# Kernel optimization log

Hardware: AMD Instinct MI355X
Metric: run time of the kernel (lower is better)

Reference implementation:

```python
import jax, jax.numpy as jnp
import numpy as np

EPS = 1e-20

def squash(s):
    # n = ||s||; out = (1 - 1/(exp(n)+eps)) * s/(n+eps)
    n = jnp.linalg.norm(s, axis=-1, keepdims=True)
    return (1.0 - 1.0 / (jnp.exp(n) + EPS)) * (s / (n + EPS))

def setup_inputs() -> dict:
    key = jax.random.key(0)
    k1, k2 = jax.random.split(key)
    B, K, J, I, Z = 128, 32, 1152, 8, 16
    x = jax.random.normal(k1, (B, J, I), dtype=jnp.float32)
    # kaiming_normal_ fan_in init for W
    W = jax.random.normal(k2, (K, J, I, Z), dtype=jnp.float32) * np.float32(np.sqrt(2.0 / (J * I)))
    b = jnp.zeros((K, J, 1), dtype=jnp.float32)
    return {"x": x, "W": W, "b": b}

def reference(x, W, b):
    Z = W.shape[-1]
    # capsule transform: u[b,k,j,z] = sum_i x[b,j,i] * W[k,j,i,z]
    u = jnp.einsum('bji,kjiz->bkjz', x, W)
    # self-similarity: c[b,k,i] = sum_{j,z} u[b,k,i,z]*u[b,k,j,z]
    #                            = sum_z u[b,k,i,z] * (sum_j u[b,k,j,z])
    c = jnp.einsum('bkjz,bkz->bkj', u, u.sum(axis=2))[..., None]
    c = c / jnp.sqrt(jnp.asarray(Z, dtype=u.dtype))
    c = jax.nn.softmax(c, axis=1) + b  # softmax over caps2 (K) axis
    s = jnp.sum(u * c, axis=-2)  # [B, K, Z]
    return squash(s)
```

## Files before the change

kernel.cpp:

```cpp
#include <hip/hip_runtime.h>
#include <hip/hip_bf16.h>
#include <math.h>

#define BB 128
#define KK 32
#define JJ 1152
#define II 8
#define ZZ 16

#define NJSA 48
#define NJT  144

typedef __attribute__((ext_vector_type(8))) short short8;
typedef __attribute__((ext_vector_type(4))) float floatx4;

#define N_USUM  (KK * BB * ZZ)
#define N_USUMP (NJSA * KK * BB * ZZ)
#define N_SACCP ((size_t)NJT * KK * BB * ZZ)

__device__ __forceinline__ float bf2f(short h) {
    unsigned int w = ((unsigned int)(unsigned short)h) << 16;
    float f; __builtin_memcpy(&f, &w, 4);
    return f;
}

extern "C" __global__ __launch_bounds__(256)
void kX(const float* __restrict__ x, __hip_bfloat16* __restrict__ xbf) {
    int idx = blockIdx.x * 256 + threadIdx.x;
    int j_in = idx & 15;
    int rest = idx >> 4;
    int b    = rest & 127;
    int j    = (rest >> 7) * 16 + j_in;
    const float4* xp = (const float4*)(x + ((size_t)b * JJ + j) * II);
    float4 a = xp[0], c = xp[1];
    union { short8 v; __hip_bfloat16 h[8]; } u;
    u.h[0] = __float2bfloat16(a.x); u.h[1] = __float2bfloat16(a.y);
    u.h[2] = __float2bfloat16(a.z); u.h[3] = __float2bfloat16(a.w);
    u.h[4] = __float2bfloat16(c.x); u.h[5] = __float2bfloat16(c.y);
    u.h[6] = __float2bfloat16(c.z); u.h[7] = __float2bfloat16(c.w);
    *(short8*)(xbf + ((size_t)j * BB + b) * II) = u.v;
}

extern "C" __global__ __launch_bounds__(256)
void kW(const float* __restrict__ W, __hip_bfloat16* __restrict__ Wt) {
    int idx = blockIdx.x * 256 + threadIdx.x;
    int z    = idx & 15;
    int rest = idx >> 4;
    int j    = rest % JJ;
    int k    = rest / JJ;
    const float* src = W + (((size_t)k * JJ + j) * II) * ZZ + z;
    union { short8 v; __hip_bfloat16 h[8]; } u;
#pragma unroll
    for (int i = 0; i < II; ++i) u.h[i] = __float2bfloat16(src[i * ZZ]);
    *(short8*)(Wt + (((size_t)k * JJ + j) * ZZ + z) * II) = u.v;
}

extern "C" __global__ __launch_bounds__(64)
void kA(const __hip_bfloat16* __restrict__ xbf,
        const __hip_bfloat16* __restrict__ Wt, float* __restrict__ usum_p) {
    const int kt = blockIdx.x;
    const int bt = blockIdx.y;
    const int js = blockIdx.z;
    const int l  = threadIdx.x;
    const int n  = l & 15;
    const int g  = l >> 4;
    const int b  = bt * 16 + n;

    short8 xv[6];
#pragma unroll
    for (int q = 0; q < 6; ++q) {
        int j = (js * 6 + q) * 4 + g;
        xv[q] = *(const short8*)(xbf + ((size_t)j * BB + b) * II);
    }

    floatx4 acc[4];
#pragma unroll
    for (int kk = 0; kk < 4; ++kk) acc[kk] = (floatx4){0.f, 0.f, 0.f, 0.f};

#pragma unroll
    for (int kk = 0; kk < 4; ++kk) {
        const int k = kt * 4 + kk;
#pragma unroll
        for (int q = 0; q < 6; ++q) {
            int j = (js * 6 + q) * 4 + g;
            short8 a = *(const short8*)(Wt + (((size_t)k * JJ + j) * ZZ + n) * II);
            acc[kk] = __builtin_amdgcn_mfma_f32_16x16x32_bf16(a, xv[q], acc[kk], 0, 0, 0);
        }
    }
#pragma unroll
    for (int kk = 0; kk < 4; ++kk) {
        const int k = kt * 4 + kk;
        *(floatx4*)(usum_p + (((size_t)js * KK + k) * BB + b) * ZZ + g * 4) = acc[kk];
    }
}

extern "C" __global__ __launch_bounds__(256)
void kR(const float* __restrict__ usum_p, float* __restrict__ usum) {
    int idx = blockIdx.x * 256 + threadIdx.x;
    floatx4 s = (floatx4){0.f, 0.f, 0.f, 0.f};
#pragma unroll 8
    for (int js = 0; js < NJSA; ++js)
        s += *(const floatx4*)(usum_p + (size_t)js * N_USUM + (size_t)idx * 4);
    *(floatx4*)(usum + (size_t)idx * 4) = s;
}

extern "C" __global__ __launch_bounds__(256)
void kBC(const __hip_bfloat16* __restrict__ xbf,
         const __hip_bfloat16* __restrict__ Wt,
         const float* __restrict__ usum, const float* __restrict__ bias,
         float* __restrict__ sacc_p) {
    __shared__ float eS[KK * 8 * 16];
    __shared__ float Sw[4 * 8 * 16];
    __shared__ float rS[8 * 16];

    const int jt = blockIdx.x;
    const int bt = blockIdx.y;
    const int t  = threadIdx.x;
    const int w  = t >> 6;
    const int l  = t & 63;
    const int n  = l & 15;
    const int g  = l >> 4;
    const int b  = bt * 16 + n;
    const int j0 = jt * 8;

    short8 xv[8];
#pragma unroll
    for (int jl = 0; jl < 8; ++jl)
        xv[jl] = *(const short8*)(xbf + ((size_t)(j0 + jl) * BB + b) * II);

    float Sacc[8];
#pragma unroll
    for (int jl = 0; jl < 8; ++jl) Sacc[jl] = 0.f;

#pragma unroll 2
    for (int kk = 0; kk < 8; ++kk) {
        const int k = w * 8 + kk;
        floatx4 us = *(const floatx4*)(usum + ((size_t)k * BB + b) * ZZ + g * 4);
#pragma unroll
        for (int jl = 0; jl < 8; ++jl) {
            short8 a = *(const short8*)(Wt + (((size_t)k * JJ + j0 + jl) * ZZ + n) * II);
            floatx4 c0 = {0.f, 0.f, 0.f, 0.f};
            floatx4 u4 = __builtin_amdgcn_mfma_f32_16x16x32_bf16(a, xv[jl], c0, 0, 0, 0);
            float dp = u4[0] * us[0];
            dp = fmaf(u4[1], us[1], dp);
            dp = fmaf(u4[2], us[2], dp);
            dp = fmaf(u4[3], us[3], dp);
            dp += __shfl_xor(dp, 16);
            dp += __shfl_xor(dp, 32);
            float e = __expf(dp * 0.0625f);
            Sacc[jl] += e;
            if (g == 0) eS[(k * 8 + jl) * 16 + n] = e;
        }
    }
    if (g == 0) {
#pragma unroll
        for (int jl = 0; jl < 8; ++jl) Sw[(w * 8 + jl) * 16 + n] = Sacc[jl];
    }
    __syncthreads();
    if (t < 128) {
        int jl = t >> 4, n2 = t & 15;
        float s = Sw[(0 * 8 + jl) * 16 + n2] + Sw[(1 * 8 + jl) * 16 + n2]
                + Sw[(2 * 8 + jl) * 16 + n2] + Sw[(3 * 8 + jl) * 16 + n2];
        rS[jl * 16 + n2] = __builtin_amdgcn_rcpf(s);
    }
    __syncthreads();

    float xf[2][8];
#pragma unroll
    for (int quad = 0; quad < 2; ++quad) {
        union { short8 v; short s[8]; } xr;
        xr.v = *(const short8*)(xbf + ((size_t)(j0 + quad * 4 + g) * BB + b) * II);
#pragma unroll
        for (int i = 0; i < II; ++i) xf[quad][i] = bf2f(xr.s[i]);
    }

    floatx4 acc[8];
#pragma unroll
    for (int kk = 0; kk < 8; ++kk) acc[kk] = (floatx4){0.f, 0.f, 0.f, 0.f};

#pragma unroll 2
    for (int kk = 0; kk < 8; ++kk) {
        const int k = w * 8 + kk;
#pragma unroll
        for (int quad = 0; quad < 2; ++quad) {
            const int jl = quad * 4 + g;
            const int j  = j0 + jl;
            float e  = eS[(k * 8 + jl) * 16 + n];
            float c  = fmaf(e, rS[jl * 16 + n], bias[(size_t)k * JJ + j]);
            union { short8 v; short s[8]; } xs;
#pragma unroll
            for (int i = 0; i < II; ++i) {
                __hip_bfloat16 hv = __float2bfloat16(xf[quad][i] * c);
                __builtin_memcpy(&xs.s[i], &hv, 2);
            }
            short8 a = *(const short8*)(Wt + (((size_t)k * JJ + j) * ZZ + n) * II);
            acc[kk] = __builtin_amdgcn_mfma_f32_16x16x32_bf16(a, xs.v, acc[kk], 0, 0, 0);
        }
    }
#pragma unroll
    for (int kk = 0; kk < 8; ++kk) {
        const int k = w * 8 + kk;
        *(floatx4*)(sacc_p + (((size_t)jt * KK + k) * BB + b) * ZZ + g * 4) = acc[kk];
    }
}

extern "C" __global__ __launch_bounds__(256)
void kD(const float* __restrict__ sacc_p, float* __restrict__ out) {
    int p  = blockIdx.x * 256 + threadIdx.x;
    int q  = p & 3;
    int kb = p >> 2;
    int k  = kb >> 7;
    int b  = kb & 127;

    floatx4 v = (floatx4){0.f, 0.f, 0.f, 0.f};
#pragma unroll 8
    for (int jt = 0; jt < NJT; ++jt)
        v += *(const floatx4*)(sacc_p + (((size_t)jt * KK + k) * BB + b) * ZZ + q * 4);

    float nsq = v[0] * v[0];
    nsq = fmaf(v[1], v[1], nsq);
    nsq = fmaf(v[2], v[2], nsq);
    nsq = fmaf(v[3], v[3], nsq);
    nsq += __shfl_xor(nsq, 1);
    nsq += __shfl_xor(nsq, 2);

    float nr = sqrtf(nsq);
    float scale = (1.f - 1.f / (__expf(nr) + 1e-20f)) / (nr + 1e-20f);
    floatx4 o = v * scale;
    *(floatx4*)(out + ((size_t)b * KK + k) * ZZ + q * 4) = o;
}

extern "C" void kernel_launch(void* const* d_in, const int* in_sizes, int n_in,
                              void* d_out, int out_size, void* d_ws, size_t ws_size,
                              hipStream_t stream) {
    const float* x    = (const float*)d_in[0];
    const float* W    = (const float*)d_in[1];
    const float* bias = (const float*)d_in[2];
    float*       out  = (float*)d_out;

    float* ws     = (float*)d_ws;
    float* usum   = ws;
    float* usum_p = usum + N_USUM;
    float* sacc_p = usum_p + N_USUMP;
    __hip_bfloat16* xbf = (__hip_bfloat16*)(sacc_p + N_SACCP);
    __hip_bfloat16* Wt  = xbf + (size_t)JJ * BB * II;


    kX<<<(JJ * BB) / 256, 256, 0, stream>>>(x, xbf);
    kW<<<(KK * JJ * ZZ) / 256, 256, 0, stream>>>(W, Wt);

    kA<<<dim3(8, 8, NJSA), 64, 0, stream>>>(xbf, Wt, usum_p);
    kR<<<64, 256, 0, stream>>>(usum_p, usum);
    kBC<<<dim3(NJT, 8), 256, 0, stream>>>(xbf, Wt, usum, bias, sacc_p);
    kD<<<(KK * BB * 4) / 256, 256, 0, stream>>>(sacc_p, out);
}
```

Measured before the change: 134.2 us.

## Merge conversion kernels, double batch tile in MFMA kernels, split reductions across lanes

The x and W bf16 conversion kernels are merged into one launch. kA and kBC now handle 32 batch rows per block instead of 16, so each loaded W fragment feeds two MFMAs, which halves W traffic and the grid size. The kR and kD partial-sum reductions are split across 4 lanes and combined with shuffles, raising parallelism in those small kernels. The wider batch tile adds register pressure and shared memory use, and the smaller grids may lower occupancy.

```diff
diff --git a/kernel.cpp b/kernel.cpp
--- a/kernel.cpp
+++ b/kernel.cpp
@@ -18,6 +18,9 @@
 #define N_USUMP (NJSA * KK * BB * ZZ)
 #define N_SACCP ((size_t)NJT * KK * BB * ZZ)
 
+#define KX_BLOCKS ((JJ * BB) / 256)
+#define KW_BLOCKS ((KK * JJ * ZZ) / 256)
+
 __device__ __forceinline__ float bf2f(short h) {
     unsigned int w = ((unsigned int)(unsigned short)h) << 16;
     float f; __builtin_memcpy(&f, &w, 4);
@@ -25,34 +28,34 @@
 }
 
 extern "C" __global__ __launch_bounds__(256)
-void kX(const float* __restrict__ x, __hip_bfloat16* __restrict__ xbf) {
-    int idx = blockIdx.x * 256 + threadIdx.x;
-    int j_in = idx & 15;
-    int rest = idx >> 4;
-    int b    = rest & 127;
-    int j    = (rest >> 7) * 16 + j_in;
-    const float4* xp = (const float4*)(x + ((size_t)b * JJ + j) * II);
-    float4 a = xp[0], c = xp[1];
-    union { short8 v; __hip_bfloat16 h[8]; } u;
-    u.h[0] = __float2bfloat16(a.x); u.h[1] = __float2bfloat16(a.y);
-    u.h[2] = __float2bfloat16(a.z); u.h[3] = __float2bfloat16(a.w);
-    u.h[4] = __float2bfloat16(c.x); u.h[5] = __float2bfloat16(c.y);
-    u.h[6] = __float2bfloat16(c.z); u.h[7] = __float2bfloat16(c.w);
-    *(short8*)(xbf + ((size_t)j * BB + b) * II) = u.v;
-}
-
-extern "C" __global__ __launch_bounds__(256)
-void kW(const float* __restrict__ W, __hip_bfloat16* __restrict__ Wt) {
-    int idx = blockIdx.x * 256 + threadIdx.x;
-    int z    = idx & 15;
-    int rest = idx >> 4;
-    int j    = rest % JJ;
-    int k    = rest / JJ;
-    const float* src = W + (((size_t)k * JJ + j) * II) * ZZ + z;
-    union { short8 v; __hip_bfloat16 h[8]; } u;
-#pragma unroll
-    for (int i = 0; i < II; ++i) u.h[i] = __float2bfloat16(src[i * ZZ]);
-    *(short8*)(Wt + (((size_t)k * JJ + j) * ZZ + z) * II) = u.v;
+void kP(const float* __restrict__ x, const float* __restrict__ W,
+        __hip_bfloat16* __restrict__ xbf, __hip_bfloat16* __restrict__ Wt) {
+    if (blockIdx.x < KX_BLOCKS) {
+        int idx = blockIdx.x * 256 + threadIdx.x;
+        int j_in = idx & 15;
+        int rest = idx >> 4;
+        int b    = rest & 127;
+        int j    = (rest >> 7) * 16 + j_in;
+        const float4* xp = (const float4*)(x + ((size_t)b * JJ + j) * II);
+        float4 a = xp[0], c = xp[1];
+        union { short8 v; __hip_bfloat16 h[8]; } u;
+        u.h[0] = __float2bfloat16(a.x); u.h[1] = __float2bfloat16(a.y);
+        u.h[2] = __float2bfloat16(a.z); u.h[3] = __float2bfloat16(a.w);
+        u.h[4] = __float2bfloat16(c.x); u.h[5] = __float2bfloat16(c.y);
+        u.h[6] = __float2bfloat16(c.z); u.h[7] = __float2bfloat16(c.w);
+        *(short8*)(xbf + ((size_t)j * BB + b) * II) = u.v;
+    } else {
+        int idx = (blockIdx.x - KX_BLOCKS) * 256 + threadIdx.x;
+        int z    = idx & 15;
+        int rest = idx >> 4;
+        int j    = rest % JJ;
+        int k    = rest / JJ;
+        const float* src = W + (((size_t)k * JJ + j) * II) * ZZ + z;
+        union { short8 v; __hip_bfloat16 h[8]; } u;
+#pragma unroll
+        for (int i = 0; i < II; ++i) u.h[i] = __float2bfloat16(src[i * ZZ]);
+        *(short8*)(Wt + (((size_t)k * JJ + j) * ZZ + z) * II) = u.v;
+    }
 }
 
 extern "C" __global__ __launch_bounds__(64)
@@ -64,18 +67,23 @@
     const int l  = threadIdx.x;
     const int n  = l & 15;
     const int g  = l >> 4;
-    const int b  = bt * 16 + n;
-
-    short8 xv[6];
+    const int b1 = bt * 32 + n;
+    const int b2 = b1 + 16;
+
+    short8 xv1[6], xv2[6];
 #pragma unroll
     for (int q = 0; q < 6; ++q) {
         int j = (js * 6 + q) * 4 + g;
-        xv[q] = *(const short8*)(xbf + ((size_t)j * BB + b) * II);
-    }
-
-    floatx4 acc[4];
-#pragma unroll
-    for (int kk = 0; kk < 4; ++kk) acc[kk] = (floatx4){0.f, 0.f, 0.f, 0.f};
+        xv1[q] = *(const short8*)(xbf + ((size_t)j * BB + b1) * II);
+        xv2[q] = *(const short8*)(xbf + ((size_t)j * BB + b2) * II);
+    }
+
+    floatx4 acc1[4], acc2[4];
+#pragma unroll
+    for (int kk = 0; kk < 4; ++kk) {
+        acc1[kk] = (floatx4){0.f, 0.f, 0.f, 0.f};
+        acc2[kk] = (floatx4){0.f, 0.f, 0.f, 0.f};
+    }
 
 #pragma unroll
     for (int kk = 0; kk < 4; ++kk) {
@@ -84,24 +92,33 @@
         for (int q = 0; q < 6; ++q) {
             int j = (js * 6 + q) * 4 + g;
             short8 a = *(const short8*)(Wt + (((size_t)k * JJ + j) * ZZ + n) * II);
-            acc[kk] = __builtin_amdgcn_mfma_f32_16x16x32_bf16(a, xv[q], acc[kk], 0, 0, 0);
+            acc1[kk] = __builtin_amdgcn_mfma_f32_16x16x32_bf16(a, xv1[q], acc1[kk], 0, 0, 0);
+            acc2[kk] = __builtin_amdgcn_mfma_f32_16x16x32_bf16(a, xv2[q], acc2[kk], 0, 0, 0);
         }
     }
 #pragma unroll
     for (int kk = 0; kk < 4; ++kk) {
         const int k = kt * 4 + kk;
-        *(floatx4*)(usum_p + (((size_t)js * KK + k) * BB + b) * ZZ + g * 4) = acc[kk];
+        *(floatx4*)(usum_p + (((size_t)js * KK + k) * BB + b1) * ZZ + g * 4) = acc1[kk];
+        *(floatx4*)(usum_p + (((size_t)js * KK + k) * BB + b2) * ZZ + g * 4) = acc2[kk];
     }
 }
 
 extern "C" __global__ __launch_bounds__(256)
 void kR(const float* __restrict__ usum_p, float* __restrict__ usum) {
-    int idx = blockIdx.x * 256 + threadIdx.x;
+    int p   = blockIdx.x * 256 + threadIdx.x;
+    int r   = p & 3;
+    int idx = p >> 2;
     floatx4 s = (floatx4){0.f, 0.f, 0.f, 0.f};
-#pragma unroll 8
-    for (int js = 0; js < NJSA; ++js)
+#pragma unroll 4
+    for (int js = r * 12; js < r * 12 + 12; ++js)
         s += *(const floatx4*)(usum_p + (size_t)js * N_USUM + (size_t)idx * 4);
-    *(floatx4*)(usum + (size_t)idx * 4) = s;
+#pragma unroll
+    for (int c = 0; c < 4; ++c) {
+        s[c] += __shfl_xor(s[c], 1);
+        s[c] += __shfl_xor(s[c], 2);
+    }
+    if (r == 0) *(floatx4*)(usum + (size_t)idx * 4) = s;
 }
 
 extern "C" __global__ __launch_bounds__(256)
@@ -109,9 +126,9 @@
          const __hip_bfloat16* __restrict__ Wt,
          const float* __restrict__ usum, const float* __restrict__ bias,
          float* __restrict__ sacc_p) {
-    __shared__ float eS[KK * 8 * 16];
-    __shared__ float Sw[4 * 8 * 16];
-    __shared__ float rS[8 * 16];
+    __shared__ float eS[KK * 8 * 32];
+    __shared__ float Sw[4 * 8 * 32];
+    __shared__ float rS[8 * 32];
 
     const int jt = blockIdx.x;
     const int bt = blockIdx.y;
@@ -120,63 +137,90 @@
     const int l  = t & 63;
     const int n  = l & 15;
     const int g  = l >> 4;
-    const int b  = bt * 16 + n;
+    const int b1 = bt * 32 + n;
+    const int b2 = b1 + 16;
     const int j0 = jt * 8;
 
-    short8 xv[8];
-#pragma unroll
-    for (int jl = 0; jl < 8; ++jl)
-        xv[jl] = *(const short8*)(xbf + ((size_t)(j0 + jl) * BB + b) * II);
-
-    float Sacc[8];
-#pragma unroll
-    for (int jl = 0; jl < 8; ++jl) Sacc[jl] = 0.f;
+    short8 xv1[8], xv2[8];
+#pragma unroll
+    for (int jl = 0; jl < 8; ++jl) {
+        xv1[jl] = *(const short8*)(xbf + ((size_t)(j0 + jl) * BB + b1) * II);
+        xv2[jl] = *(const short8*)(xbf + ((size_t)(j0 + jl) * BB + b2) * II);
+    }
+
+    float Sacc1[8], Sacc2[8];
+#pragma unroll
+    for (int jl = 0; jl < 8; ++jl) { Sacc1[jl] = 0.f; Sacc2[jl] = 0.f; }
 
 #pragma unroll 2
     for (int kk = 0; kk < 8; ++kk) {
         const int k = w * 8 + kk;
-        floatx4 us = *(const floatx4*)(usum + ((size_t)k * BB + b) * ZZ + g * 4);
+        floatx4 us1 = *(const floatx4*)(usum + ((size_t)k * BB + b1) * ZZ + g * 4);
+        floatx4 us2 = *(const floatx4*)(usum + ((size_t)k * BB + b2) * ZZ + g * 4);
 #pragma unroll
         for (int jl = 0; jl < 8; ++jl) {
             short8 a = *(const short8*)(Wt + (((size_t)k * JJ + j0 + jl) * ZZ + n) * II);
             floatx4 c0 = {0.f, 0.f, 0.f, 0.f};
-            floatx4 u4 = __builtin_amdgcn_mfma_f32_16x16x32_bf16(a, xv[jl], c0, 0, 0, 0);
-            float dp = u4[0] * us[0];
-            dp = fmaf(u4[1], us[1], dp);
-            dp = fmaf(u4[2], us[2], dp);
-            dp = fmaf(u4[3], us[3], dp);
-            dp += __shfl_xor(dp, 16);
-            dp += __shfl_xor(dp, 32);
-            float e = __expf(dp * 0.0625f);
-            Sacc[jl] += e;
-            if (g == 0) eS[(k * 8 + jl) * 16 + n] = e;
+            floatx4 u1 = __builtin_amdgcn_mfma_f32_16x16x32_bf16(a, xv1[jl], c0, 0, 0, 0);
+            floatx4 u2 = __builtin_amdgcn_mfma_f32_16x16x32_bf16(a, xv2[jl], c0, 0, 0, 0);
+            float dp1 = u1[0] * us1[0];
+            dp1 = fmaf(u1[1], us1[1], dp1);
+            dp1 = fmaf(u1[2], us1[2], dp1);
+            dp1 = fmaf(u1[3], us1[3], dp1);
+            float dp2 = u2[0] * us2[0];
+            dp2 = fmaf(u2[1], us2[1], dp2);
+            dp2 = fmaf(u2[2], us2[2], dp2);
+            dp2 = fmaf(u2[3], us2[3], dp2);
+            dp1 += __shfl_xor(dp1, 16);
+            dp1 += __shfl_xor(dp1, 32);
+            dp2 += __shfl_xor(dp2, 16);
+            dp2 += __shfl_xor(dp2, 32);
+            float e1 = __expf(dp1 * 0.0625f);
+            float e2 = __expf(dp2 * 0.0625f);
+            Sacc1[jl] += e1;
+            Sacc2[jl] += e2;
+            if (g == 0) {
+                eS[(k * 8 + jl) * 32 + n]      = e1;
+                eS[(k * 8 + jl) * 32 + n + 16] = e2;
+            }
         }
     }
     if (g == 0) {
 #pragma unroll
-        for (int jl = 0; jl < 8; ++jl) Sw[(w * 8 + jl) * 16 + n] = Sacc[jl];
+        for (int jl = 0; jl < 8; ++jl) {
+            Sw[(w * 8 + jl) * 32 + n]      = Sacc1[jl];
+            Sw[(w * 8 + jl) * 32 + n + 16] = Sacc2[jl];
+        }
     }
     __syncthreads();
-    if (t < 128) {
-        int jl = t >> 4, n2 = t & 15;
-        float s = Sw[(0 * 8 + jl) * 16 + n2] + Sw[(1 * 8 + jl) * 16 + n2]
-                + Sw[(2 * 8 + jl) * 16 + n2] + Sw[(3 * 8 + jl) * 16 + n2];
-        rS[jl * 16 + n2] = __builtin_amdgcn_rcpf(s);
+    {
+        int jl = t >> 5, col = t & 31;
+        float s = Sw[(0 * 8 + jl) * 32 + col] + Sw[(1 * 8 + jl) * 32 + col]
+                + Sw[(2 * 8 + jl) * 32 + col] + Sw[(3 * 8 + jl) * 32 + col];
+        rS[jl * 32 + col] = __builtin_amdgcn_rcpf(s);
     }
     __syncthreads();
 
-    float xf[2][8];
+    float xf1[2][8], xf2[2][8];
 #pragma unroll
     for (int quad = 0; quad < 2; ++quad) {
-        union { short8 v; short s[8]; } xr;
-        xr.v = *(const short8*)(xbf + ((size_t)(j0 + quad * 4 + g) * BB + b) * II);
-#pragma unroll
-        for (int i = 0; i < II; ++i) xf[quad][i] = bf2f(xr.s[i]);
-    }
-
-    floatx4 acc[8];
-#pragma unroll
-    for (int kk = 0; kk < 8; ++kk) acc[kk] = (floatx4){0.f, 0.f, 0.f, 0.f};
+        union { short8 v; short s[8]; } xr1, xr2;
+        int j = j0 + quad * 4 + g;
+        xr1.v = *(const short8*)(xbf + ((size_t)j * BB + b1) * II);
+        xr2.v = *(const short8*)(xbf + ((size_t)j * BB + b2) * II);
+#pragma unroll
+        for (int i = 0; i < II; ++i) {
+            xf1[quad][i] = bf2f(xr1.s[i]);
+            xf2[quad][i] = bf2f(xr2.s[i]);
+        }
+    }
+
+    floatx4 acc1[8], acc2[8];
+#pragma unroll
+    for (int kk = 0; kk < 8; ++kk) {
+        acc1[kk] = (floatx4){0.f, 0.f, 0.f, 0.f};
+        acc2[kk] = (floatx4){0.f, 0.f, 0.f, 0.f};
+    }
 
 #pragma unroll 2
     for (int kk = 0; kk < 8; ++kk) {
@@ -185,49 +229,63 @@
         for (int quad = 0; quad < 2; ++quad) {
             const int jl = quad * 4 + g;
             const int j  = j0 + jl;
-            float e  = eS[(k * 8 + jl) * 16 + n];
-            float c  = fmaf(e, rS[jl * 16 + n], bias[(size_t)k * JJ + j]);
-            union { short8 v; short s[8]; } xs;
+            float bj = bias[(size_t)k * JJ + j];
+            float c1 = fmaf(eS[(k * 8 + jl) * 32 + n],      rS[jl * 32 + n],      bj);
+            float c2 = fmaf(eS[(k * 8 + jl) * 32 + n + 16], rS[jl * 32 + n + 16], bj);
+            union { short8 v; short s[8]; } xs1, xs2;
 #pragma unroll
             for (int i = 0; i < II; ++i) {
-                __hip_bfloat16 hv = __float2bfloat16(xf[quad][i] * c);
-                __builtin_memcpy(&xs.s[i], &hv, 2);
+                __hip_bfloat16 h1 = __float2bfloat16(xf1[quad][i] * c1);
+                __hip_bfloat16 h2 = __float2bfloat16(xf2[quad][i] * c2);
+                __builtin_memcpy(&xs1.s[i], &h1, 2);
+                __builtin_memcpy(&xs2.s[i], &h2, 2);
             }
             short8 a = *(const short8*)(Wt + (((size_t)k * JJ + j) * ZZ + n) * II);
-            acc[kk] = __builtin_amdgcn_mfma_f32_16x16x32_bf16(a, xs.v, acc[kk], 0, 0, 0);
+            acc1[kk] = __builtin_amdgcn_mfma_f32_16x16x32_bf16(a, xs1.v, acc1[kk], 0, 0, 0);
+            acc2[kk] = __builtin_amdgcn_mfma_f32_16x16x32_bf16(a, xs2.v, acc2[kk], 0, 0, 0);
         }
     }
 #pragma unroll
     for (int kk = 0; kk < 8; ++kk) {
         const int k = w * 8 + kk;
-        *(floatx4*)(sacc_p + (((size_t)jt * KK + k) * BB + b) * ZZ + g * 4) = acc[kk];
+        *(floatx4*)(sacc_p + (((size_t)jt * KK + k) * BB + b1) * ZZ + g * 4) = acc1[kk];
+        *(floatx4*)(sacc_p + (((size_t)jt * KK + k) * BB + b2) * ZZ + g * 4) = acc2[kk];
     }
 }
 
 extern "C" __global__ __launch_bounds__(256)
 void kD(const float* __restrict__ sacc_p, float* __restrict__ out) {
     int p  = blockIdx.x * 256 + threadIdx.x;
-    int q  = p & 3;
-    int kb = p >> 2;
+    int r  = p & 3;
+    int q  = (p >> 2) & 3;
+    int kb = p >> 4;
     int k  = kb >> 7;
     int b  = kb & 127;
 
     floatx4 v = (floatx4){0.f, 0.f, 0.f, 0.f};
-#pragma unroll 8
-    for (int jt = 0; jt < NJT; ++jt)
+#pragma unroll 6
+    for (int jt = r * 36; jt < r * 36 + 36; ++jt)
         v += *(const floatx4*)(sacc_p + (((size_t)jt * KK + k) * BB + b) * ZZ + q * 4);
+
+#pragma unroll
+    for (int c = 0; c < 4; ++c) {
+        v[c] += __shfl_xor(v[c], 1);
+        v[c] += __shfl_xor(v[c], 2);
+    }
 
     float nsq = v[0] * v[0];
     nsq = fmaf(v[1], v[1], nsq);
     nsq = fmaf(v[2], v[2], nsq);
     nsq = fmaf(v[3], v[3], nsq);
-    nsq += __shfl_xor(nsq, 1);
-    nsq += __shfl_xor(nsq, 2);
+    nsq += __shfl_xor(nsq, 4);
+    nsq += __shfl_xor(nsq, 8);
 
     float nr = sqrtf(nsq);
     float scale = (1.f - 1.f / (__expf(nr) + 1e-20f)) / (nr + 1e-20f);
-    floatx4 o = v * scale;
-    *(floatx4*)(out + ((size_t)b * KK + k) * ZZ + q * 4) = o;
+    if (r == 0) {
+        floatx4 o = v * scale;
+        *(floatx4*)(out + ((size_t)b * KK + k) * ZZ + q * 4) = o;
+    }
 }
 
 extern "C" void kernel_launch(void* const* d_in, const int* in_sizes, int n_in,
@@ -246,11 +304,9 @@
     __hip_bfloat16* Wt  = xbf + (size_t)JJ * BB * II;
 
 
-    kX<<<(JJ * BB) / 256, 256, 0, stream>>>(x, xbf);
-    kW<<<(KK * JJ * ZZ) / 256, 256, 0, stream>>>(W, Wt);
-
-    kA<<<dim3(8, 8, NJSA), 64, 0, stream>>>(xbf, Wt, usum_p);
-    kR<<<64, 256, 0, stream>>>(usum_p, usum);
-    kBC<<<dim3(NJT, 8), 256, 0, stream>>>(xbf, Wt, usum, bias, sacc_p);
-    kD<<<(KK * BB * 4) / 256, 256, 0, stream>>>(sacc_p, out);
-}
+    kP<<<KX_BLOCKS + KW_BLOCKS, 256, 0, stream>>>(x, W, xbf, Wt);
+    kA<<<dim3(8, 4, NJSA), 64, 0, stream>>>(xbf, Wt, usum_p);
+    kR<<<(KK * BB * ZZ) / 256, 256, 0, stream>>>(usum_p, usum);
+    kBC<<<dim3(NJT, 4), 256, 0, stream>>>(xbf, Wt, usum, bias, sacc_p);
+    kD<<<(KK * BB * 16) / 256, 256, 0, stream>>>(sacc_p, out);
+}
```

Result: no change. 132.4 us (-1.3%).
